# Optimization experiments

Hardware: AMD Instinct MI355X
Metric: run time of the kernel (lower is better)

The kernel has to match this reference:

```python
import jax, jax.numpy as jnp
import numpy as np
from jax import lax


def squash(s):
    # scale = |s|^2/(1+|s|^2); out = scale * s/|s| (eps-stabilized as in source)
    norm = jnp.sum(s * s, axis=-1, keepdims=True)
    return (norm / (1.0 + norm)) * (s / jnp.sqrt(norm + 1e-8))


def setup_inputs() -> dict:
    key = jax.random.key(0)
    k = jax.random.split(key, 4)
    B, H, C = 32, 64, 10
    x = jax.random.normal(k[0], (B, 3, H, H), jnp.float32)
    conv1_w = jax.random.normal(k[1], (256, 3, 9, 9), jnp.float32) * 0.06
    conv1_b = jnp.zeros((256,), jnp.float32)
    conv2_w = jax.random.normal(k[2], (256, 256, 9, 9), jnp.float32) * 0.02  # 256 = 8 caps * 32 routes
    conv2_b = jnp.zeros((256,), jnp.float32)
    route_w = jax.random.normal(k[3], (32, C, 8, 16), jnp.float32)  # [routes, classes, in_dim, out_dim]
    return {"x": x, "conv1_w": conv1_w, "conv1_b": conv1_b,
            "conv2_w": conv2_w, "conv2_b": conv2_b, "route_w": route_w}


def reference(x, conv1_w, conv1_b, conv2_w, conv2_b, route_w):
    dn = ("NCHW", "OIHW", "NCHW")
    # PrimaryCapsules: conv 3->256 k9 s1 + relu
    h = lax.conv_general_dilated(x, conv1_w, (1, 1), "VALID", dimension_numbers=dn)
    h = jax.nn.relu(h + conv1_b[None, :, None, None])
    # CapsuleLayer conv: 256 -> 8*32 k9 s2
    h = lax.conv_general_dilated(h, conv2_w, (2, 2), "VALID", dimension_numbers=dn)
    h = h + conv2_b[None, :, None, None]
    B, _, hh, ww = h.shape
    R, D = 32, 8  # num_routes, capsule dim
    # [B, R*D, h, w] -> [B, R, P, D], squash per capsule vector
    caps = h.reshape(B, R, D, hh, ww).transpose(0, 1, 3, 4, 2).reshape(B, R, hh * ww, D)
    caps = squash(caps)
    # DigitCapsules: per-route linear maps 8->16, shared over spatial positions
    u_hat = jnp.einsum("brpi,rcio->brpco", caps, route_w)  # [B, R, P, C, 16]
    C, O = u_hat.shape[3], u_hat.shape[4]
    u_hat = u_hat.reshape(B, R * hh * ww, C, O)  # [B, N, C, 16]
    b_log = jnp.zeros(u_hat.shape[:-1], u_hat.dtype)  # [B, N, C]
    num_routing = 3
    v = None
    for i in range(num_routing):
        c = jax.nn.softmax(b_log, axis=2)            # over classes (dim=2 in source)
        s = jnp.einsum("bnc,bnco->bco", c, u_hat)    # weighted sum over input caps
        v = squash(s)                                 # [B, C, 16]
        if i < num_routing - 1:
            b_log = b_log + jnp.einsum("bnco,bco->bnc", u_hat, v)  # agreement
    return v
```

## Files before the change

kernel.cpp:

```cpp
#include <hip/hip_runtime.h>
#include <hip/hip_bf16.h>
#include <stdint.h>

typedef __attribute__((ext_vector_type(8))) short short8;
typedef __attribute__((ext_vector_type(4))) float f32x4;
typedef unsigned int u32x4a __attribute__((vector_size(16)));
typedef unsigned int u32x4u __attribute__((vector_size(16), aligned(4)));

__device__ inline unsigned short f2bf(float f) {
    union { float f; uint32_t u; } v; v.f = f;
    uint32_t u = v.u;
    uint32_t r = (u + 0x7FFFu + ((u >> 16) & 1u)) >> 16;
    return (unsigned short)r;
}

__device__ inline void gl_lds16(const unsigned short* g, unsigned short* l) {
    __builtin_amdgcn_global_load_lds(
        (const uint32_t __attribute__((address_space(1)))*)(const void*)g,
        (uint32_t __attribute__((address_space(3)))*)(void*)l, 16, 0, 0);
}

__global__ void cvt_w1(const float* __restrict__ w, unsigned short* __restrict__ A1) {
    int idx = blockIdx.x * 256 + threadIdx.x;
    int row = idx >> 8, k = idx & 255;
    float v = (k < 243) ? w[row * 243 + k] : 0.f;
    A1[idx] = f2bf(v);
}

__global__ void cvt_w2(const float* __restrict__ w, unsigned short* __restrict__ A2t) {
    int idx = blockIdx.x * 256 + threadIdx.x;
    int j = idx & 7;
    int off16 = (idx >> 3) & 1023;
    int tile = idx >> 13;
    int tm = tile / 324, chunk = tile - tm * 324;
    int row = off16 >> 3, sw = off16 & 7;
    int koct = sw ^ (row & 7);
    int kk = chunk * 64 + koct * 8 + j;
    int oc = tm * 128 + row;
    int ic, ky, kx;
    if (kk < 18432) { ic = kk / 72; int rem = kk - ic * 72; ky = rem >> 3; kx = rem & 7; }
    else { int j2 = kk - 18432; ic = j2 / 9; ky = j2 - ic * 9; kx = 8; }
    A2t[idx] = f2bf(w[((oc * 256 + ic) * 9 + ky) * 9 + kx]);
}

__global__ __launch_bounds__(256) void conv1_gemm(
    const unsigned short* __restrict__ A,
    const float* __restrict__ x,
    const float* __restrict__ bias,
    unsigned short* __restrict__ h1)
{
    __shared__ __align__(16) unsigned short As[128 * 40];
    __shared__ __align__(16) unsigned short Bs[128 * 40];
    const int tid = threadIdx.x;
    const int m0 = blockIdx.y * 128;
    const int n0 = blockIdx.x * 128;
    const int lane = tid & 63;
    const int wave = tid >> 6;
    const int wy = wave & 1, wx = wave >> 1;
    const int l16 = lane & 15, q = lane >> 4;

    const int kp = tid & 15;
    const int gn = tid >> 4;
    int baseN[8];
#pragma unroll
    for (int j = 0; j < 8; ++j) {
        int n = n0 + gn * 8 + j;
        int b = n / 3136, p = n % 3136;
        int oy = p / 56, ox = p % 56;
        baseN[j] = b * 12288 + oy * 64 + ox;
    }

    f32x4 acc[4][4];
#pragma unroll
    for (int im = 0; im < 4; ++im)
#pragma unroll
        for (int in = 0; in < 4; ++in)
            acc[im][in] = (f32x4){0.f, 0.f, 0.f, 0.f};

    for (int k0 = 0; k0 < 256; k0 += 32) {
        __syncthreads();
#pragma unroll
        for (int s = 0; s < 2; ++s) {
            int slot = tid + s * 256;
            int row = slot >> 2, seg = slot & 3;
            u32x4a v = *(const u32x4a*)(A + (m0 + row) * 256 + k0 + seg * 8);
            *(u32x4a*)(&As[row * 40 + seg * 8]) = v;
        }
        int ka = k0 + 2 * kp, kb = ka + 1;
        int offa = 0, offb = 0;
        bool va = ka < 243, vb = kb < 243;
        if (va) { int c = ka / 81, t = ka % 81, ky = t / 9, kx = t % 9; offa = c * 4096 + ky * 64 + kx; }
        if (vb) { int c = kb / 81, t = kb % 81, ky = t / 9, kx = t % 9; offb = c * 4096 + ky * 64 + kx; }
#pragma unroll
        for (int j = 0; j < 8; ++j) {
            unsigned int ba = va ? (unsigned int)f2bf(x[baseN[j] + offa]) : 0u;
            unsigned int bb = vb ? (unsigned int)f2bf(x[baseN[j] + offb]) : 0u;
            *(unsigned int*)(&Bs[(gn * 8 + j) * 40 + 2 * kp]) = ba | (bb << 16);
        }
        __syncthreads();

        short8 af[4], bf[4];
#pragma unroll
        for (int im = 0; im < 4; ++im)
            af[im] = *(const short8*)(&As[(wy * 64 + im * 16 + l16) * 40 + q * 8]);
#pragma unroll
        for (int in = 0; in < 4; ++in)
            bf[in] = *(const short8*)(&Bs[(wx * 64 + in * 16 + l16) * 40 + q * 8]);
#pragma unroll
        for (int im = 0; im < 4; ++im)
#pragma unroll
            for (int in = 0; in < 4; ++in)
                acc[im][in] = __builtin_amdgcn_mfma_f32_16x16x32_bf16(af[im], bf[in], acc[im][in], 0, 0, 0);
    }

#pragma unroll
    for (int in = 0; in < 4; ++in) {
        int n = n0 + wx * 64 + in * 16 + l16;
        int b = n / 3136, p = n % 3136;
        int oy = p / 56, ox = p % 56;
#pragma unroll
        for (int im = 0; im < 4; ++im) {
#pragma unroll
            for (int r = 0; r < 4; ++r) {
                int oc = m0 + wy * 64 + im * 16 + q * 4 + r;
                float v = acc[im][in][r] + bias[oc];
                v = v > 0.f ? v : 0.f;
                h1[((b * 256 + oc) * 56 + oy) * 56 + ox] = f2bf(v);
            }
        }
    }
}

#define C2ROW 72
__global__ __launch_bounds__(256) void conv2_gemm(
    const unsigned short* __restrict__ A2t,
    const unsigned short* __restrict__ h1,
    float* __restrict__ c2)
{
    __shared__ __align__(16) unsigned short As[2][8192];
    __shared__ __align__(16) unsigned short Bs[128 * C2ROW];
    const int tid = threadIdx.x;
    const int n0 = blockIdx.x * 128;
    const int z = blockIdx.z;
    const int lane = tid & 63;
    const int wave = tid >> 6;
    const int wy = wave & 1, wx = wave >> 1;
    const int l16 = lane & 15, q = lane >> 4;

    const int oct = tid >> 5;
    int bsrc[4], bdst[4];
#pragma unroll
    for (int i = 0; i < 4; ++i) {
        int n = (tid & 31) + 32 * i;
        int ng = n0 + n;
        int b = ng / 576, p = ng % 576;
        int oy = p / 24, ox = p % 24;
        bsrc[i] = b * 802816 + (2 * oy) * 56 + 2 * ox;
        bdst[i] = n * C2ROW + oct * 8;
    }
    const int tn = tid & 127, thalf = tid >> 7;
    int tbase;
    {
        int ng = n0 + tn;
        int b = ng / 576, p = ng % 576;
        int oy = p / 24, ox = p % 24;
        tbase = b * 802816 + (2 * oy) * 56 + 2 * ox + 8;
    }

    f32x4 acc[4][4];
#pragma unroll
    for (int im = 0; im < 4; ++im)
#pragma unroll
        for (int in = 0; in < 4; ++in)
            acc[im][in] = (f32x4){0.f, 0.f, 0.f, 0.f};

    const size_t tilebase = (size_t)blockIdx.y * 324 * 8192;
    uint32_t bR[16];

    auto issueA = [&](int c, int buf) {
        const unsigned short* at = A2t + tilebase + (size_t)c * 8192;
        int s0 = wave * 4;
#pragma unroll
        for (int i = 0; i < 4; ++i) {
            int sl = (s0 + i) * 64 + lane;
            gl_lds16(at + sl * 8, &As[buf][sl * 8]);
        }
    };
    auto loadB = [&](int c) {
        if (c < 288) {
            int octk = c * 8 + oct;
            int ic = octk / 9, ky = octk - ic * 9;
            int off = ic * 3136 + ky * 56;
#pragma unroll
            for (int i = 0; i < 4; ++i) {
                u32x4u v = *(const u32x4u*)(h1 + bsrc[i] + off);
                bR[4 * i + 0] = v[0]; bR[4 * i + 1] = v[1];
                bR[4 * i + 2] = v[2]; bR[4 * i + 3] = v[3];
            }
        } else {
            int base = c * 64 + thalf * 32 - 18432;
#pragma unroll
            for (int p = 0; p < 16; ++p) {
                int j2 = base + 2 * p;
                int icA = j2 / 9, kyA = j2 - icA * 9;
                int icB = (j2 + 1) / 9, kyB = (j2 + 1) - icB * 9;
                uint32_t ba = h1[tbase + icA * 3136 + kyA * 56];
                uint32_t bb = h1[tbase + icB * 3136 + kyB * 56];
                bR[p] = ba | (bb << 16);
            }
        }
    };
    auto writeB = [&](int c) {
        if (c < 288) {
#pragma unroll
            for (int i = 0; i < 4; ++i) {
                u32x4a v = {bR[4 * i], bR[4 * i + 1], bR[4 * i + 2], bR[4 * i + 3]};
                *(u32x4a*)(&Bs[bdst[i]]) = v;
            }
        } else {
#pragma unroll
            for (int p = 0; p < 16; ++p)
                *(uint32_t*)(&Bs[tn * C2ROW + thalf * 32 + 2 * p]) = bR[p];
        }
    };

    const int nch = (324 - z + 7) >> 3;
    int c = z;
    issueA(c, 0);
    loadB(c);
    for (int i = 0; i < nch; ++i) {
        const int cur = i & 1;
        const int ccur = c, cnext = c + 8;
        __asm__ volatile("s_waitcnt vmcnt(0)" ::: "memory");
        __syncthreads();
        writeB(ccur);
        __syncthreads();
        if (i + 1 < nch) { issueA(cnext, cur ^ 1); loadB(cnext); }
#pragma unroll
        for (int h = 0; h < 2; ++h) {
            short8 af[4], bf[4];
#pragma unroll
            for (int im = 0; im < 4; ++im) {
                int row = wy * 64 + im * 16 + l16;
                int koct = h * 4 + q;
                af[im] = *(const short8*)(&As[cur][(row * 8 + (koct ^ (row & 7))) * 8]);
            }
#pragma unroll
            for (int in = 0; in < 4; ++in)
                bf[in] = *(const short8*)(&Bs[(wx * 64 + in * 16 + l16) * C2ROW + h * 32 + q * 8]);
#pragma unroll
            for (int im = 0; im < 4; ++im)
#pragma unroll
                for (int in = 0; in < 4; ++in)
                    acc[im][in] = __builtin_amdgcn_mfma_f32_16x16x32_bf16(af[im], bf[in], acc[im][in], 0, 0, 0);
        }
        c = cnext;
    }

    const int m0 = blockIdx.y * 128;
#pragma unroll
    for (int in = 0; in < 4; ++in) {
        int nn = n0 + wx * 64 + in * 16 + l16;
        int bb = nn / 576, pp = nn % 576;
#pragma unroll
        for (int im = 0; im < 4; ++im) {
#pragma unroll
            for (int r = 0; r < 4; ++r) {
                int oc = m0 + wy * 64 + im * 16 + q * 4 + r;
                atomicAdd(&c2[(bb * 256 + oc) * 576 + pp], acc[im][in][r]);
            }
        }
    }
}

__global__ void squash_caps(const float* __restrict__ c2, const float* __restrict__ bias,
                            float* __restrict__ caps) {
    int idx = blockIdx.x * 256 + threadIdx.x;
    int b = idx / 18432;
    int rp = idx % 18432;
    int r = rp / 576, p = rp % 576;
    float s[8]; float n2 = 0.f;
#pragma unroll
    for (int d = 0; d < 8; ++d) {
        s[d] = c2[(b * 256 + r * 8 + d) * 576 + p] + bias[r * 8 + d];
        n2 += s[d] * s[d];
    }
    float sc = (n2 / (1.f + n2)) / sqrtf(n2 + 1e-8f);
#pragma unroll
    for (int d = 0; d < 8; ++d)
        caps[idx * 8 + d] = sc * s[d];
}

__global__ __launch_bounds__(64) void capsum0(const float* __restrict__ caps,
                                              float* __restrict__ G) {
    int r = blockIdx.x, b = blockIdx.y;
    const float* cp = caps + (size_t)(b * 32 + r) * 4608;
    int tid = threadIdx.x;
    f32x4 s0 = (f32x4){0.f, 0.f, 0.f, 0.f}, s1 = s0;
    for (int jv = 0; jv < 9; ++jv) {
        const f32x4* qp = (const f32x4*)(cp + (jv * 64 + tid) * 8);
        s0 += qp[0]; s1 += qp[1];
    }
#pragma unroll
    for (int off = 32; off > 0; off >>= 1) {
#pragma unroll
        for (int k = 0; k < 4; ++k) {
            s0[k] += __shfl_down(s0[k], off, 64);
            s1[k] += __shfl_down(s1[k], off, 64);
        }
    }
    if (tid == 0) {
        float g[8] = {s0[0], s0[1], s0[2], s0[3], s1[0], s1[1], s1[2], s1[3]};
        float* gp = G + (size_t)((b * 32 + r) * 10) * 8;
        for (int cc = 0; cc < 10; ++cc)
#pragma unroll
            for (int ii = 0; ii < 8; ++ii) gp[cc * 8 + ii] = g[ii] * 0.1f;
    }
}

__global__ __launch_bounds__(64) void route_accum(const float* __restrict__ caps,
                                                  const float* __restrict__ W,
                                                  const float* __restrict__ V,
                                                  float* __restrict__ G) {
    int r = blockIdx.x, b = blockIdx.y;
    __shared__ float wv[80];
    __shared__ float red[80][64];
    int tid = threadIdx.x;
    for (int v = tid; v < 80; v += 64) {
        int cc = v >> 3, ii = v & 7;
        float s = 0.f;
#pragma unroll
        for (int o = 0; o < 16; ++o)
            s += W[((r * 10 + cc) * 8 + ii) * 16 + o] * V[(b * 10 + cc) * 16 + o];
        wv[v] = s;
    }
    __syncthreads();
    float g[80];
#pragma unroll
    for (int v = 0; v < 80; ++v) g[v] = 0.f;
    const float* cp = caps + (size_t)(b * 32 + r) * 4608;
    for (int j = 0; j < 9; ++j) {
        int p = j * 64 + tid;
        const f32x4* qp = (const f32x4*)(cp + p * 8);
        f32x4 c0 = qp[0], c1 = qp[1];
        float c8[8];
#pragma unroll
        for (int i = 0; i < 4; ++i) { c8[i] = c0[i]; c8[4 + i] = c1[i]; }
        float a[10]; float m = -1e30f;
#pragma unroll
        for (int cc = 0; cc < 10; ++cc) {
            float t = 0.f;
#pragma unroll
            for (int i = 0; i < 8; ++i) t += c8[i] * wv[cc * 8 + i];
            a[cc] = t; m = fmaxf(m, t);
        }
        float sum = 0.f;
#pragma unroll
        for (int cc = 0; cc < 10; ++cc) { a[cc] = __expf(a[cc] - m); sum += a[cc]; }
        float inv = 1.f / sum;
#pragma unroll
        for (int cc = 0; cc < 10; ++cc) {
            float w = a[cc] * inv;
#pragma unroll
            for (int i = 0; i < 8; ++i) g[cc * 8 + i] += w * c8[i];
        }
    }
#pragma unroll
    for (int v = 0; v < 80; ++v) red[v][tid] = g[v];
    __syncthreads();
    for (int v = tid; v < 80; v += 64) {
        float s = 0.f;
        for (int t = 0; t < 64; ++t) s += red[v][t];
        G[(b * 32 + r) * 80 + v] = s;
    }
}

__global__ __launch_bounds__(160) void sv_kernel(const float* __restrict__ G,
                                                 const float* __restrict__ W,
                                                 float* __restrict__ V,
                                                 float* __restrict__ out, int last) {
    int b = blockIdx.x;
    int c = threadIdx.x / 16, o = threadIdx.x % 16;
    __shared__ float sL[10][16];
    float s = 0.f;
    for (int r = 0; r < 32; ++r) {
        const float* g = G + ((b * 32 + r) * 10 + c) * 8;
        const float* w = W + ((r * 10 + c) * 8) * 16 + o;
#pragma unroll
        for (int i = 0; i < 8; ++i) s += g[i] * w[i * 16];
    }
    sL[c][o] = s;
    __syncthreads();
    float n2 = 0.f;
#pragma unroll
    for (int oo = 0; oo < 16; ++oo) { float t = sL[c][oo]; n2 += t * t; }
    float sc = (n2 / (1.f + n2)) / sqrtf(n2 + 1e-8f);
    float v = sc * s;
    V[(b * 10 + c) * 16 + o] += v;
    if (last) out[(b * 10 + c) * 16 + o] = v;
}

extern "C" void kernel_launch(void* const* d_in, const int* in_sizes, int n_in,
                              void* d_out, int out_size, void* d_ws, size_t ws_size,
                              hipStream_t stream) {
    const float* x  = (const float*)d_in[0];
    const float* w1 = (const float*)d_in[1];
    const float* b1 = (const float*)d_in[2];
    const float* w2 = (const float*)d_in[3];
    const float* b2 = (const float*)d_in[4];
    const float* rw = (const float*)d_in[5];

    char* ws = (char*)d_ws;
    unsigned short* A1   = (unsigned short*)(ws);
    unsigned short* A2   = (unsigned short*)(ws + 262144);
    unsigned short* h1   = (unsigned short*)(ws + 10878976);
    float*          c2   = (float*)(ws + 62259200);
    float*          caps = (float*)(ws + 81133568);
    float*          V    = (float*)(ws + 100007936);
    float*          G    = (float*)(ws + 100028416);

    hipLaunchKernelGGL(cvt_w1, dim3(256), dim3(256), 0, stream, w1, A1);
    hipLaunchKernelGGL(cvt_w2, dim3(20736), dim3(256), 0, stream, w2, A2);
    hipMemsetAsync(c2, 0, 18874368, stream);
    hipLaunchKernelGGL(conv1_gemm, dim3(784, 2), dim3(256), 0, stream, A1, x, b1, h1);
    hipLaunchKernelGGL(conv2_gemm, dim3(144, 2, 8), dim3(256), 0, stream, A2, h1, c2);
    hipLaunchKernelGGL(squash_caps, dim3(2304), dim3(256), 0, stream, c2, b2, caps);
    hipMemsetAsync(V, 0, 5120 * sizeof(float), stream);
    hipLaunchKernelGGL(capsum0, dim3(32, 32), dim3(64), 0, stream, caps, G);
    hipLaunchKernelGGL(sv_kernel, dim3(32), dim3(160), 0, stream, G, rw, V, (float*)d_out, 0);
    for (int it = 1; it < 3; ++it) {
        hipLaunchKernelGGL(route_accum, dim3(32, 32), dim3(64), 0, stream, caps, rw, V, G);
        hipLaunchKernelGGL(sv_kernel, dim3(32), dim3(160), 0, stream, G, rw, V,
                           (float*)d_out, it == 2 ? 1 : 0);
    }
}
```

Before: 470.6 us.

## Stream conv2 B tile straight into double-buffered LDS with async loads

The im2col B tile for the main conv2 K-range is now fetched with global_load_lds straight into a second, double-buffered LDS array. This replaces the register load followed by an LDS write and one barrier per chunk, and the B layout becomes k-octet-major to match the 16-byte async transfers. The irregular tail chunks still go through registers and keep an extra barrier. The explicit vmcnt wait before the barrier is removed, so correctness depends on the barrier waiting for the async LDS loads. LDS use grows with the second B buffer.

```diff
diff --git a/kernel.cpp b/kernel.cpp
--- a/kernel.cpp
+++ b/kernel.cpp
@@ -131,14 +131,13 @@
     }
 }
 
-#define C2ROW 72
 __global__ __launch_bounds__(256) void conv2_gemm(
     const unsigned short* __restrict__ A2t,
     const unsigned short* __restrict__ h1,
     float* __restrict__ c2)
 {
     __shared__ __align__(16) unsigned short As[2][8192];
-    __shared__ __align__(16) unsigned short Bs[128 * C2ROW];
+    __shared__ __align__(16) unsigned short Bs[2][8192];
     const int tid = threadIdx.x;
     const int n0 = blockIdx.x * 128;
     const int z = blockIdx.z;
@@ -147,24 +146,21 @@
     const int wy = wave & 1, wx = wave >> 1;
     const int l16 = lane & 15, q = lane >> 4;
 
-    const int oct = tid >> 5;
-    int bsrc[4], bdst[4];
-#pragma unroll
-    for (int i = 0; i < 4; ++i) {
-        int n = (tid & 31) + 32 * i;
-        int ng = n0 + n;
-        int b = ng / 576, p = ng % 576;
-        int oy = p / 24, ox = p % 24;
-        bsrc[i] = b * 802816 + (2 * oy) * 56 + 2 * ox;
-        bdst[i] = n * C2ROW + oct * 8;
+    int bsrcA, bsrcB;
+    {
+        int ngA = n0 + lane;
+        int bA = ngA / 576, pA = ngA % 576;
+        bsrcA = bA * 802816 + (2 * (pA / 24)) * 56 + 2 * (pA % 24);
+        int ngB = n0 + 64 + lane;
+        int bB = ngB / 576, pB = ngB % 576;
+        bsrcB = bB * 802816 + (2 * (pB / 24)) * 56 + 2 * (pB % 24);
     }
     const int tn = tid & 127, thalf = tid >> 7;
     int tbase;
     {
         int ng = n0 + tn;
         int b = ng / 576, p = ng % 576;
-        int oy = p / 24, ox = p % 24;
-        tbase = b * 802816 + (2 * oy) * 56 + 2 * ox + 8;
+        tbase = b * 802816 + (2 * (p / 24)) * 56 + 2 * (p % 24) + 8;
     }
 
     f32x4 acc[4][4];
@@ -186,56 +182,51 @@
             gl_lds16(at + sl * 8, &As[buf][sl * 8]);
         }
     };
-    auto loadB = [&](int c) {
-        if (c < 288) {
-            int octk = c * 8 + oct;
+    auto issueB = [&](int c, int buf) {
+#pragma unroll
+        for (int i = 0; i < 4; ++i) {
+            int jp = wave * 4 + i;
+            int octk = c * 8 + (jp >> 1);
             int ic = octk / 9, ky = octk - ic * 9;
-            int off = ic * 3136 + ky * 56;
-#pragma unroll
-            for (int i = 0; i < 4; ++i) {
-                u32x4u v = *(const u32x4u*)(h1 + bsrc[i] + off);
-                bR[4 * i + 0] = v[0]; bR[4 * i + 1] = v[1];
-                bR[4 * i + 2] = v[2]; bR[4 * i + 3] = v[3];
-            }
-        } else {
-            int base = c * 64 + thalf * 32 - 18432;
-#pragma unroll
-            for (int p = 0; p < 16; ++p) {
-                int j2 = base + 2 * p;
-                int icA = j2 / 9, kyA = j2 - icA * 9;
-                int icB = (j2 + 1) / 9, kyB = (j2 + 1) - icB * 9;
-                uint32_t ba = h1[tbase + icA * 3136 + kyA * 56];
-                uint32_t bb = h1[tbase + icB * 3136 + kyB * 56];
-                bR[p] = ba | (bb << 16);
-            }
+            int src = ((jp & 1) ? bsrcB : bsrcA) + ic * 3136 + ky * 56;
+            int sl = jp * 64 + lane;
+            gl_lds16(h1 + src, &Bs[buf][sl * 8]);
         }
     };
-    auto writeB = [&](int c) {
-        if (c < 288) {
-#pragma unroll
-            for (int i = 0; i < 4; ++i) {
-                u32x4a v = {bR[4 * i], bR[4 * i + 1], bR[4 * i + 2], bR[4 * i + 3]};
-                *(u32x4a*)(&Bs[bdst[i]]) = v;
-            }
-        } else {
-#pragma unroll
-            for (int p = 0; p < 16; ++p)
-                *(uint32_t*)(&Bs[tn * C2ROW + thalf * 32 + 2 * p]) = bR[p];
+    auto loadBtail = [&](int c) {
+        int base = c * 64 + thalf * 32 - 18432;
+#pragma unroll
+        for (int p = 0; p < 16; ++p) {
+            int j2 = base + 2 * p;
+            int icA = j2 / 9, kyA = j2 - icA * 9;
+            int icB = (j2 + 1) / 9, kyB = (j2 + 1) - icB * 9;
+            uint32_t ba = h1[tbase + icA * 3136 + kyA * 56];
+            uint32_t bb = h1[tbase + icB * 3136 + kyB * 56];
+            bR[p] = ba | (bb << 16);
+        }
+    };
+    auto writeBtail = [&](int buf) {
+#pragma unroll
+        for (int p = 0; p < 16; ++p) {
+            int kk = thalf * 32 + 2 * p;
+            int koct = kk >> 3, slot = kk & 7;
+            *(uint32_t*)(&Bs[buf][(koct * 128 + tn) * 8 + slot]) = bR[p];
         }
     };
 
     const int nch = (324 - z + 7) >> 3;
     int c = z;
     issueA(c, 0);
-    loadB(c);
+    if (c < 288) issueB(c, 0); else loadBtail(c);
     for (int i = 0; i < nch; ++i) {
         const int cur = i & 1;
-        const int ccur = c, cnext = c + 8;
-        __asm__ volatile("s_waitcnt vmcnt(0)" ::: "memory");
+        const int cnext = c + 8;
         __syncthreads();
-        writeB(ccur);
-        __syncthreads();
-        if (i + 1 < nch) { issueA(cnext, cur ^ 1); loadB(cnext); }
+        if (c >= 288) { writeBtail(cur); __syncthreads(); }
+        if (i + 1 < nch) {
+            issueA(cnext, cur ^ 1);
+            if (cnext < 288) issueB(cnext, cur ^ 1); else loadBtail(cnext);
+        }
 #pragma unroll
         for (int h = 0; h < 2; ++h) {
             short8 af[4], bf[4];
@@ -247,7 +238,7 @@
             }
 #pragma unroll
             for (int in = 0; in < 4; ++in)
-                bf[in] = *(const short8*)(&Bs[(wx * 64 + in * 16 + l16) * C2ROW + h * 32 + q * 8]);
+                bf[in] = *(const short8*)(&Bs[cur][((h * 4 + q) * 128 + wx * 64 + in * 16 + l16) * 8]);
 #pragma unroll
             for (int im = 0; im < 4; ++im)
 #pragma unroll
```

Measured after the change: 498.3 us. 1.06x slower.
